# Kernel tuning notes

Hardware: AMD Instinct MI355X
Metric: run time of the kernel (lower is better)

The kernel has to match this reference:

```python
import jax, jax.numpy as jnp
import numpy as np

ANCHORS = [np.array([[10, 13], [16, 30], [33, 23]], np.float32),
           np.array([[30, 61], [62, 45], [59, 119]], np.float32),
           np.array([[116, 90], [156, 198], [373, 326]], np.float32)]
STRIDES = [8.0, 16.0, 32.0]
BALANCE = [4.0, 1.0, 0.4]
LAMBDA_OBJ, LAMBDA_CLS, LAMBDA_IOU = 1.0, 0.5, 1.0
NUM_CLASSES = 80
EPS = 1e-7


def _bce_logits(x, t):
    # numerically stable BCEWithLogits, reduction='none'
    return jnp.maximum(x, 0.0) - x * t + jnp.log1p(jnp.exp(-jnp.abs(x)))


def _ciou(box1, box2):
    # boxes in (cx, cy, w, h); standard ultralytics CIoU
    w1, h1 = box1[..., 2], box1[..., 3]
    w2, h2 = box2[..., 2], box2[..., 3]
    b1x1, b1x2 = box1[..., 0] - w1 / 2, box1[..., 0] + w1 / 2
    b1y1, b1y2 = box1[..., 1] - h1 / 2, box1[..., 1] + h1 / 2
    b2x1, b2x2 = box2[..., 0] - w2 / 2, box2[..., 0] + w2 / 2
    b2y1, b2y2 = box2[..., 1] - h2 / 2, box2[..., 1] + h2 / 2
    inter = (jnp.clip(jnp.minimum(b1x2, b2x2) - jnp.maximum(b1x1, b2x1), 0.0, None)
             * jnp.clip(jnp.minimum(b1y2, b2y2) - jnp.maximum(b1y1, b2y1), 0.0, None))
    union = w1 * h1 + w2 * h2 - inter + EPS
    iou = inter / union
    cw = jnp.maximum(b1x2, b2x2) - jnp.minimum(b1x1, b2x1)  # enclosing box
    ch = jnp.maximum(b1y2, b2y2) - jnp.minimum(b1y1, b2y1)
    c2 = cw ** 2 + ch ** 2 + EPS
    rho2 = ((b2x1 + b2x2 - b1x1 - b1x2) ** 2 + (b2y1 + b2y2 - b1y1 - b1y2) ** 2) / 4.0
    v = (4.0 / np.pi ** 2) * (jnp.arctan(w2 / (h2 + EPS)) - jnp.arctan(w1 / (h1 + EPS))) ** 2
    alpha = jax.lax.stop_gradient(v / (v - iou + 1.0 + EPS))
    return iou - (rho2 / c2 + v * alpha)


def _build_targets(boxes, labels, stride, anchors_wh, B, A, H, W, C):
    # Vectorized version of the torch per-gt loops: anchor shape matching +
    # scatter into dense target tensors. boxes [B,N,4] x1y1x2y2, labels [B,N].
    gt_xy = (boxes[..., :2] + boxes[..., 2:]) / 2.0          # [B,N,2]
    gt_wh = boxes[..., 2:] - boxes[..., :2]                  # [B,N,2]
    xy_grid = gt_xy / stride
    gi = jnp.clip(xy_grid[..., 1].astype(jnp.int32), 0, H - 1)
    gj = jnp.clip(xy_grid[..., 0].astype(jnp.int32), 0, W - 1)
    r = gt_wh[:, :, None, :] / anchors_wh[None, None, :, :]  # [B,N,A,2]
    shape_metric = jnp.maximum(r[..., 0], 1.0 / r[..., 0]) * jnp.maximum(r[..., 1], 1.0 / r[..., 1])
    best = jnp.argmax(1.0 / shape_metric, axis=-1)           # [B,N]
    tx = xy_grid[..., 0] - gj.astype(jnp.float32)
    ty = xy_grid[..., 1] - gi.astype(jnp.float32)
    aw = anchors_wh[best]                                    # [B,N,2]
    tw = jnp.log(gt_wh[..., 0] / (aw[..., 0] + 1e-16))
    th = jnp.log(gt_wh[..., 1] / (aw[..., 1] + 1e-16))
    bidx = jnp.broadcast_to(jnp.arange(B)[:, None], best.shape)
    obj = jnp.zeros((B, A, H, W), jnp.float32).at[bidx, best, gi, gj].set(1.0)
    tvals = jax.lax.stop_gradient(jnp.stack([tx, ty, tw, th], axis=-1))
    tbox = jnp.zeros((B, A, H, W, 4), jnp.float32).at[bidx, best, gi, gj].set(tvals)
    tcls = jnp.zeros((B, A, H, W, C), jnp.float32).at[bidx, best, gi, gj, labels].set(1.0)
    return obj, tbox, tcls


def _scale_loss(pred, boxes, labels, anchors_raw, stride, balance):
    B, _, H, W = pred.shape
    A = anchors_raw.shape[0]
    C = NUM_CLASSES
    p = pred.reshape(B, A, 5 + C, H, W).transpose(0, 1, 3, 4, 2)  # [B,A,H,W,5+C]
    pbox, pobj, pcls = p[..., :4], p[..., 4], p[..., 5:]
    gy, gx = jnp.meshgrid(jnp.arange(H, dtype=jnp.float32),
                          jnp.arange(W, dtype=jnp.float32), indexing='ij')
    grid = jnp.stack([gx, gy], axis=-1)                           # [H,W,2]
    anchors = jnp.asarray(anchors_raw)
    anchors_wh = anchors * stride                                  # pixel-space anchors
    pred_xy = (jax.nn.sigmoid(pbox[..., :2]) + grid) * stride
    pred_wh = jnp.exp(pbox[..., 2:]) * anchors_wh[None, :, None, None, :]
    pred_boxes = jnp.concatenate([pred_xy, pred_wh], axis=-1)      # cxcywh pixels
    obj, tbox, tcls = _build_targets(boxes, labels, stride, anchors_wh, B, A, H, W, C)
    npos = jnp.sum(obj)
    # decode target boxes back to cxcywh pixels (matches indices-based torch path)
    tgt_xy = (grid + tbox[..., :2]) * stride
    tgt_wh = jnp.exp(tbox[..., 2:]) * anchors_wh[None, :, None, None, :]
    tgt_boxes = jnp.concatenate([tgt_xy, tgt_wh], axis=-1)
    ciou = _ciou(pred_boxes, tgt_boxes)
    box_l = LAMBDA_IOU * jnp.sum((1.0 - ciou) * obj) / jnp.maximum(npos, 1.0)
    bce_obj = _bce_logits(pobj, obj)  # positive target = 1, negative target = 0
    obj_l = LAMBDA_OBJ * balance * (jnp.sum(bce_obj * obj) + 0.5 * jnp.sum(bce_obj * (1.0 - obj)))
    cls_l = LAMBDA_CLS * jnp.sum(_bce_logits(pcls, tcls) * obj[..., None])
    return box_l, obj_l, cls_l


def setup_inputs() -> dict:
    key = jax.random.key(0)
    k1, k2, k3, k4, k5, k6 = jax.random.split(key, 6)
    B, N, C, A = 16, 32, 80, 3
    ch = A * (5 + C)
    pred_small = jax.random.normal(k1, (B, ch, 80, 80), jnp.float32)
    pred_medium = jax.random.normal(k2, (B, ch, 40, 40), jnp.float32)
    pred_large = jax.random.normal(k3, (B, ch, 20, 20), jnp.float32)
    cxy = jax.random.uniform(k4, (B, N, 2), minval=32.0, maxval=608.0)
    wh = jax.random.uniform(k5, (B, N, 2), minval=8.0, maxval=256.0)
    boxes = jnp.concatenate([cxy - wh / 2, cxy + wh / 2], axis=-1)  # x1y1x2y2, 640px img
    labels = jax.random.randint(k6, (B, N), 0, C)
    return {"pred_small": pred_small, "pred_medium": pred_medium,
            "pred_large": pred_large, "boxes": boxes, "labels": labels}


def reference(pred_small, pred_medium, pred_large, boxes, labels):
    B = pred_small.shape[0]
    box_l = obj_l = cls_l = jnp.float32(0.0)
    for pred, anc, stride, bal in zip((pred_small, pred_medium, pred_large), ANCHORS, STRIDES, BALANCE):
        b, o, c = _scale_loss(pred, boxes, labels, anc, stride, bal)
        box_l, obj_l, cls_l = box_l + b, obj_l + o, cls_l + c
    total = (box_l + obj_l + cls_l) / B
    return total
```

## Files before the change

### kernel.cpp

```cpp
#include <hip/hip_runtime.h>
#include <math.h>

#define EPSF 1e-7f

__constant__ float c_anch[3][3][2] = {
    {{80.f,104.f},{128.f,240.f},{264.f,184.f}},
    {{480.f,976.f},{992.f,720.f},{944.f,1904.f}},
    {{3712.f,2880.f},{4992.f,6336.f},{11936.f,10432.f}}
};
__constant__ float c_stride[3] = {8.f, 16.f, 32.f};
__constant__ float c_bal[3]    = {4.f, 1.f, 0.4f};
__constant__ int   c_HW[3]     = {6400, 1600, 400};
__constant__ int   c_W[3]      = {80, 40, 20};

__device__ __forceinline__ float bce0(float x) {
    return fmaxf(x, 0.f) + __logf(1.f + __expf(-fabsf(x)));
}

__global__ __launch_bounds__(256) void fused_main(
        const float* __restrict__ p0, const float* __restrict__ p1,
        const float* __restrict__ p2,
        const float* __restrict__ boxes, const int* __restrict__ labels,
        float4* __restrict__ part, float* __restrict__ nposPart)
{
    __shared__ float red[4][4];

    const int bid  = blockIdx.x;
    const int tid  = threadIdx.x;
    const int lane = tid & 63, wv = tid >> 6;

    const bool isPos = (bid < 384);
    const int s   = bid >> 7;
    const int b   = (bid >> 3) & 15;
    const int grp = bid & 7;

    float4 bx; int labl = 0;
    if (isPos && lane < 32) {
        bx   = ((const float4*)boxes)[b * 32 + lane];
        labl = labels[b * 32 + lane];
    }

    float dsum = 0.f;
    {
        int v = bid * 252 + tid;
        if (tid < 252) {
            int sc, run, off, HW;
            const float* pred;
            if (v < 76800)      { sc = 0; HW = 6400; run = v / 1600;          off = v - run * 1600;         pred = p0; }
            else if (v < 96000) { sc = 1; HW = 1600; int u = v - 76800; run = u / 400; off = u - run * 400; pred = p1; }
            else                { sc = 2; HW = 400;  int u = v - 96000; run = u / 100; off = u - run * 100; pred = p2; }
            int bb = run / 3, a = run - bb * 3;
            const float4* ptr = (const float4*)(pred + (size_t)(bb * 255 + a * 85 + 4) * HW) + off;
            float4 x = *ptr;
            float w = 0.5f * c_bal[sc];
            dsum = w * (bce0(x.x) + bce0(x.y) + bce0(x.z) + bce0(x.w));
        }
    }

    float boxc = 0.f, objc = 0.f, clsp = 0.f;
    if (isPos) {
        int key = 0; float txl = 0.f, tyl = 0.f, twl = 0.f, thl = 0.f;
        {
            float cx = (bx.x + bx.z) * 0.5f, cy = (bx.y + bx.w) * 0.5f;
            float w  = bx.z - bx.x,          h  = bx.w - bx.y;
            float stride = c_stride[s];
            float xg = cx / stride, yg = cy / stride;
            int W = c_W[s];
            int gi = min(max((int)yg, 0), W - 1);
            int gj = min(max((int)xg, 0), W - 1);
            int best = 0; float bm = 1e30f;
            for (int k = 0; k < 3; ++k) {
                float aw = c_anch[s][k][0], ah = c_anch[s][k][1];
                float r0 = w / aw, r1 = h / ah;
                float m = fmaxf(r0, 1.f / r0) * fmaxf(r1, 1.f / r1);
                if (m < bm) { bm = m; best = k; }
            }
            float aw = c_anch[s][best][0], ah = c_anch[s][best][1];
            key = (best << 20) | (gi << 10) | gj;
            txl = xg - (float)gj;
            tyl = yg - (float)gi;
            twl = __logf(w / (aw + 1e-16f));
            thl = __logf(h / (ah + 1e-16f));
        }

        if (grp == 0 && wv == 0) {
            bool dup = false;
            for (int d = 1; d < 32; ++d) {
                int nk = __shfl(key, (lane + d) & 31);
                dup |= ((lane + d) < 32) && (nk == key);
            }
            bool winl = (lane < 32) && !dup;
            unsigned long long bal = __ballot(winl);
            if (lane == 0) nposPart[s * 16 + b] = (float)__popcll(bal);
        }

        const int n = grp * 4 + wv;
        int   key_n = __shfl(key, n);
        float tx_n  = __shfl(txl, n);
        float ty_n  = __shfl(tyl, n);
        float tw_n  = __shfl(twl, n);
        float th_n  = __shfl(thl, n);
        int   lab   = __shfl(labl, n);
        unsigned long long dupm =
            __ballot((lane > n) && (lane < 32) && (key == key_n));
        bool win = (dupm == 0ull);

        if (win) {
            int a  = key_n >> 20;
            int gi = (key_n >> 10) & 1023;
            int gj = key_n & 1023;
            const int HW = c_HW[s], W = c_W[s];
            int hw = gi * W + gj;
            const float* pred = (s == 0) ? p0 : ((s == 1) ? p1 : p2);
            const float* pb_ = pred + (size_t)(b * 255 + a * 85) * HW + hw;
            const float* pc  = pb_ + (size_t)5 * HW;

            float xc0 = pc[(size_t)lane * HW];
            float xc1 = (lane < 16) ? pc[(size_t)(lane + 64) * HW] : 0.f;
            clsp = bce0(xc0) - ((lane == lab) ? xc0 : 0.f);
            if (lane < 16) clsp += bce0(xc1) - ((lane + 64 == lab) ? xc1 : 0.f);

            float px = pb_[0], py = pb_[(size_t)HW];
            float pw = pb_[2 * (size_t)HW], ph = pb_[3 * (size_t)HW];
            float xo = pb_[4 * (size_t)HW];

            objc = c_bal[s] * (0.5f * bce0(xo) - xo);

            const float stride = c_stride[s];
            const float aw = c_anch[s][a][0], ah = c_anch[s][a][1];
            float sx = 1.f / (1.f + __expf(-px));
            float sy = 1.f / (1.f + __expf(-py));
            float b1x = (sx + (float)gj) * stride, b1y = (sy + (float)gi) * stride;
            float b1w = __expf(pw) * aw,           b1h = __expf(ph) * ah;
            float b2x = ((float)gj + tx_n) * stride, b2y = ((float)gi + ty_n) * stride;
            float b2w = __expf(tw_n) * aw,           b2h = __expf(th_n) * ah;

            float b1x1 = b1x - b1w * 0.5f, b1x2 = b1x + b1w * 0.5f;
            float b1y1 = b1y - b1h * 0.5f, b1y2 = b1y + b1h * 0.5f;
            float b2x1 = b2x - b2w * 0.5f, b2x2 = b2x + b2w * 0.5f;
            float b2y1 = b2y - b2h * 0.5f, b2y2 = b2y + b2h * 0.5f;
            float iw = fmaxf(fminf(b1x2, b2x2) - fmaxf(b1x1, b2x1), 0.f);
            float ih = fmaxf(fminf(b1y2, b2y2) - fmaxf(b1y1, b2y1), 0.f);
            float inter = iw * ih;
            float uni = b1w * b1h + b2w * b2h - inter + EPSF;
            float iou = inter / uni;
            float cwv = fmaxf(b1x2, b2x2) - fminf(b1x1, b2x1);
            float chv = fmaxf(b1y2, b2y2) - fminf(b1y1, b2y1);
            float c2 = cwv * cwv + chv * chv + EPSF;
            float dx = b2x1 + b2x2 - b1x1 - b1x2;
            float dy = b2y1 + b2y2 - b1y1 - b1y2;
            float rho2 = (dx * dx + dy * dy) * 0.25f;
            float dat = atanf(b2w / (b2h + EPSF)) - atanf(b1w / (b1h + EPSF));
            float v = (4.f / (float)(M_PI * M_PI)) * dat * dat;
            float alpha = v / (v - iou + 1.f + EPSF);
            boxc = 1.f - (iou - (rho2 / c2 + v * alpha));
        }
    }

    for (int o = 32; o > 0; o >>= 1) {
        dsum += __shfl_down(dsum, o);
        clsp += __shfl_down(clsp, o);
    }
    if (lane == 0) {
        red[wv][0] = dsum; red[wv][1] = boxc; red[wv][2] = objc; red[wv][3] = clsp;
    }
    __syncthreads();
    if (tid == 0) {
        float d = 0.f, bxs = 0.f, oc = 0.f, cl = 0.f;
        for (int i = 0; i < 4; ++i) {
            d += red[i][0]; bxs += red[i][1]; oc += red[i][2]; cl += red[i][3];
        }
        part[bid] = make_float4(bxs, d + oc, cl, 0.f);
    }
}

__global__ __launch_bounds__(256) void finalize(
        const float4* __restrict__ part, const float* __restrict__ nposPart,
        float* __restrict__ out)
{
    int tid = threadIdx.x;
    float bx0 = 0.f, bx1 = 0.f, bx2 = 0.f, obj = 0.f, cls = 0.f;
    for (int i = tid; i < 400; i += 256) {
        float4 p = part[i];
        obj += p.y;
        cls += p.z;
        int sc = i >> 7;
        bx0 += (sc == 0) ? p.x : 0.f;
        bx1 += (sc == 1) ? p.x : 0.f;
        bx2 += (sc == 2) ? p.x : 0.f;
    }
    float np0 = 0.f, np1 = 0.f, np2 = 0.f;
    if (tid < 48) {
        float v = nposPart[tid];
        int sc = tid / 16;
        np0 = (sc == 0) ? v : 0.f;
        np1 = (sc == 1) ? v : 0.f;
        np2 = (sc == 2) ? v : 0.f;
    }

    for (int o = 32; o > 0; o >>= 1) {
        bx0 += __shfl_down(bx0, o);
        bx1 += __shfl_down(bx1, o);
        bx2 += __shfl_down(bx2, o);
        obj += __shfl_down(obj, o);
        cls += __shfl_down(cls, o);
        np0 += __shfl_down(np0, o);
        np1 += __shfl_down(np1, o);
        np2 += __shfl_down(np2, o);
    }
    __shared__ float red[4][8];
    int wv = tid >> 6;
    if ((tid & 63) == 0) {
        red[wv][0] = bx0; red[wv][1] = bx1; red[wv][2] = bx2; red[wv][3] = obj;
        red[wv][4] = cls; red[wv][5] = np0; red[wv][6] = np1; red[wv][7] = np2;
    }
    __syncthreads();
    if (tid == 0) {
        float v[8];
        for (int j = 0; j < 8; ++j)
            v[j] = red[0][j] + red[1][j] + red[2][j] + red[3][j];
        float tot = v[0] / fmaxf(v[5], 1.f)
                  + v[1] / fmaxf(v[6], 1.f)
                  + v[2] / fmaxf(v[7], 1.f)
                  + v[3]
                  + 0.5f * v[4];
        out[0] = tot / 16.f;
    }
}

extern "C" void kernel_launch(void* const* d_in, const int* in_sizes, int n_in,
                              void* d_out, int out_size, void* d_ws, size_t ws_size,
                              hipStream_t stream)
{
    const float* p0     = (const float*)d_in[0];
    const float* p1     = (const float*)d_in[1];
    const float* p2     = (const float*)d_in[2];
    const float* boxes  = (const float*)d_in[3];
    const int*   labels = (const int*)d_in[4];

    char* ws = (char*)d_ws;
    float4* part     = (float4*)ws;
    float*  nposPart = (float*)(ws + 6656);

    fused_main<<<400, 256, 0, stream>>>(p0, p1, p2, boxes, labels,
                                        part, nposPart);
    finalize<<<1, 256, 0, stream>>>(part, nposPart, (float*)d_out);
}
```

Measured before the change: 12.12 us.

## Fuse finalize into main kernel via per-block npos recompute and atomicAdd

Removes the second finalize launch. Each positive block now recomputes the per-scale count of unique positive cells for all 16 images itself: each wave handles 4 images, two per half-wave, with redundant key building. Each block then adds its normalized contribution to the output with atomicAdd after a memset. This trades a kernel launch and an inter-kernel dependency for duplicated dedup work in every positive block, atomic contention on a single float, and a nondeterministic summation order.

Measured after the change: 20.23 us. 67.0% more time.

```diff
diff --git a/kernel.cpp b/kernel.cpp
--- a/kernel.cpp
+++ b/kernel.cpp
@@ -17,13 +17,30 @@
     return fmaxf(x, 0.f) + __logf(1.f + __expf(-fabsf(x)));
 }
 
-__global__ __launch_bounds__(256) void fused_main(
+__device__ __forceinline__ int buildKey(float4 bx, int s) {
+    float cx = (bx.x + bx.z) * 0.5f, cy = (bx.y + bx.w) * 0.5f;
+    float w  = bx.z - bx.x,          h  = bx.w - bx.y;
+    float stride = c_stride[s];
+    int W = c_W[s];
+    int gi = min(max((int)(cy / stride), 0), W - 1);
+    int gj = min(max((int)(cx / stride), 0), W - 1);
+    int best = 0; float bm = 1e30f;
+    for (int k = 0; k < 3; ++k) {
+        float aw = c_anch[s][k][0], ah = c_anch[s][k][1];
+        float r0 = w / aw, r1 = h / ah;
+        float m = fmaxf(r0, 1.f / r0) * fmaxf(r1, 1.f / r1);
+        if (m < bm) { bm = m; best = k; }
+    }
+    return (best << 20) | (gi << 10) | gj;
+}
+
+__global__ __launch_bounds__(256) void fused_all(
         const float* __restrict__ p0, const float* __restrict__ p1,
         const float* __restrict__ p2,
         const float* __restrict__ boxes, const int* __restrict__ labels,
-        float4* __restrict__ part, float* __restrict__ nposPart)
+        float* __restrict__ out)
 {
-    __shared__ float red[4][4];
+    __shared__ float red[4][5];
 
     const int bid  = blockIdx.x;
     const int tid  = threadIdx.x;
@@ -35,9 +52,14 @@
     const int grp = bid & 7;
 
     float4 bx; int labl = 0;
-    if (isPos && lane < 32) {
-        bx   = ((const float4*)boxes)[b * 32 + lane];
-        labl = labels[b * 32 + lane];
+    float4 bxn0, bxn1;
+    if (isPos) {
+        if (lane < 32) {
+            bx   = ((const float4*)boxes)[b * 32 + lane];
+            labl = labels[b * 32 + lane];
+        }
+        bxn0 = ((const float4*)boxes)[(wv * 4 + 0 + (lane >> 5)) * 32 + (lane & 31)];
+        bxn1 = ((const float4*)boxes)[(wv * 4 + 2 + (lane >> 5)) * 32 + (lane & 31)];
     }
 
     float dsum = 0.f;
@@ -58,7 +80,26 @@
     }
 
     float boxc = 0.f, objc = 0.f, clsp = 0.f;
+    float npw = 0.f;
     if (isPos) {
+        {
+            const int l32 = lane & 31, base = lane & 32;
+            int k0 = buildKey(bxn0, s);
+            bool dup = false;
+            for (int d = 1; d < 32; ++d) {
+                int nk = __shfl(k0, base + ((l32 + d) & 31));
+                dup |= ((l32 + d) < 32) && (nk == k0);
+            }
+            npw += (float)__popcll(__ballot(!dup));
+            int k1 = buildKey(bxn1, s);
+            dup = false;
+            for (int d = 1; d < 32; ++d) {
+                int nk = __shfl(k1, base + ((l32 + d) & 31));
+                dup |= ((l32 + d) < 32) && (nk == k1);
+            }
+            npw += (float)__popcll(__ballot(!dup));
+        }
+
         int key = 0; float txl = 0.f, tyl = 0.f, twl = 0.f, thl = 0.f;
         {
             float cx = (bx.x + bx.z) * 0.5f, cy = (bx.y + bx.w) * 0.5f;
@@ -83,17 +124,6 @@
             thl = __logf(h / (ah + 1e-16f));
         }
 
-        if (grp == 0 && wv == 0) {
-            bool dup = false;
-            for (int d = 1; d < 32; ++d) {
-                int nk = __shfl(key, (lane + d) & 31);
-                dup |= ((lane + d) < 32) && (nk == key);
-            }
-            bool winl = (lane < 32) && !dup;
-            unsigned long long bal = __ballot(winl);
-            if (lane == 0) nposPart[s * 16 + b] = (float)__popcll(bal);
-        }
-
         const int n = grp * 4 + wv;
         int   key_n = __shfl(key, n);
         float tx_n  = __shfl(txl, n);
@@ -162,69 +192,18 @@
         clsp += __shfl_down(clsp, o);
     }
     if (lane == 0) {
-        red[wv][0] = dsum; red[wv][1] = boxc; red[wv][2] = objc; red[wv][3] = clsp;
+        red[wv][0] = dsum; red[wv][1] = boxc; red[wv][2] = objc;
+        red[wv][3] = clsp; red[wv][4] = npw;
     }
     __syncthreads();
     if (tid == 0) {
-        float d = 0.f, bxs = 0.f, oc = 0.f, cl = 0.f;
+        float d = 0.f, bxs = 0.f, oc = 0.f, cl = 0.f, np = 0.f;
         for (int i = 0; i < 4; ++i) {
-            d += red[i][0]; bxs += red[i][1]; oc += red[i][2]; cl += red[i][3];
-        }
-        part[bid] = make_float4(bxs, d + oc, cl, 0.f);
-    }
-}
-
-__global__ __launch_bounds__(256) void finalize(
-        const float4* __restrict__ part, const float* __restrict__ nposPart,
-        float* __restrict__ out)
-{
-    int tid = threadIdx.x;
-    float bx0 = 0.f, bx1 = 0.f, bx2 = 0.f, obj = 0.f, cls = 0.f;
-    for (int i = tid; i < 400; i += 256) {
-        float4 p = part[i];
-        obj += p.y;
-        cls += p.z;
-        int sc = i >> 7;
-        bx0 += (sc == 0) ? p.x : 0.f;
-        bx1 += (sc == 1) ? p.x : 0.f;
-        bx2 += (sc == 2) ? p.x : 0.f;
-    }
-    float np0 = 0.f, np1 = 0.f, np2 = 0.f;
-    if (tid < 48) {
-        float v = nposPart[tid];
-        int sc = tid / 16;
-        np0 = (sc == 0) ? v : 0.f;
-        np1 = (sc == 1) ? v : 0.f;
-        np2 = (sc == 2) ? v : 0.f;
-    }
-
-    for (int o = 32; o > 0; o >>= 1) {
-        bx0 += __shfl_down(bx0, o);
-        bx1 += __shfl_down(bx1, o);
-        bx2 += __shfl_down(bx2, o);
-        obj += __shfl_down(obj, o);
-        cls += __shfl_down(cls, o);
-        np0 += __shfl_down(np0, o);
-        np1 += __shfl_down(np1, o);
-        np2 += __shfl_down(np2, o);
-    }
-    __shared__ float red[4][8];
-    int wv = tid >> 6;
-    if ((tid & 63) == 0) {
-        red[wv][0] = bx0; red[wv][1] = bx1; red[wv][2] = bx2; red[wv][3] = obj;
-        red[wv][4] = cls; red[wv][5] = np0; red[wv][6] = np1; red[wv][7] = np2;
-    }
-    __syncthreads();
-    if (tid == 0) {
-        float v[8];
-        for (int j = 0; j < 8; ++j)
-            v[j] = red[0][j] + red[1][j] + red[2][j] + red[3][j];
-        float tot = v[0] / fmaxf(v[5], 1.f)
-                  + v[1] / fmaxf(v[6], 1.f)
-                  + v[2] / fmaxf(v[7], 1.f)
-                  + v[3]
-                  + 0.5f * v[4];
-        out[0] = tot / 16.f;
+            d  += red[i][0]; bxs += red[i][1]; oc += red[i][2];
+            cl += red[i][3]; np  += red[i][4];
+        }
+        float contrib = d + oc + 0.5f * cl + bxs / fmaxf(np, 1.f);
+        atomicAdd(out, contrib * 0.0625f);
     }
 }
 
@@ -238,11 +217,8 @@
     const float* boxes  = (const float*)d_in[3];
     const int*   labels = (const int*)d_in[4];
 
-    char* ws = (char*)d_ws;
-    float4* part     = (float4*)ws;
-    float*  nposPart = (float*)(ws + 6656);
-
-    fused_main<<<400, 256, 0, stream>>>(p0, p1, p2, boxes, labels,
-                                        part, nposPart);
-    finalize<<<1, 256, 0, stream>>>(part, nposPart, (float*)d_out);
-}
+    hipMemsetAsync(d_out, 0, sizeof(float), stream);
+
+    fused_all<<<400, 256, 0, stream>>>(p0, p1, p2, boxes, labels,
+                                       (float*)d_out);
+}
```

## Fuse finalize into main kernel via last-block epoch-tagged spin wait

Applied to the files above, without the earlier changes.

Removes the separate finalize launch. Each block publishes its partials with agent-scope atomic stores and bumps a per-block tag with release semantics. Block 399 waits until every tag reaches the current epoch, then does the final reduction. This saves one kernel launch and its gap, but it relies on all 400 blocks being resident or completing before block 399 spins, and it adds atomic traffic.

Result: slower. 15.26 us (+25.9%).

```diff
diff --git a/kernel.cpp b/kernel.cpp
--- a/kernel.cpp
+++ b/kernel.cpp
@@ -13,17 +13,29 @@
 __constant__ int   c_HW[3]     = {6400, 1600, 400};
 __constant__ int   c_W[3]      = {80, 40, 20};
 
+__device__ unsigned int g_tag[400];
+__device__ unsigned int g_epoch;
+
 __device__ __forceinline__ float bce0(float x) {
     return fmaxf(x, 0.f) + __logf(1.f + __expf(-fabsf(x)));
 }
 
-__global__ __launch_bounds__(256) void fused_main(
+__device__ __forceinline__ void agent_store(float* p, float v) {
+    __hip_atomic_store(p, v, __ATOMIC_RELAXED, __HIP_MEMORY_SCOPE_AGENT);
+}
+__device__ __forceinline__ float agent_load(const float* p) {
+    return __hip_atomic_load(p, __ATOMIC_RELAXED, __HIP_MEMORY_SCOPE_AGENT);
+}
+
+__global__ __launch_bounds__(256) void fused_all(
         const float* __restrict__ p0, const float* __restrict__ p1,
         const float* __restrict__ p2,
         const float* __restrict__ boxes, const int* __restrict__ labels,
-        float4* __restrict__ part, float* __restrict__ nposPart)
+        float* __restrict__ part, float* __restrict__ nposPart,
+        float* __restrict__ out)
 {
-    __shared__ float red[4][4];
+    __shared__ float red[4][8];
+    __shared__ unsigned int sEpoch;
 
     const int bid  = blockIdx.x;
     const int tid  = threadIdx.x;
@@ -91,7 +103,7 @@
             }
             bool winl = (lane < 32) && !dup;
             unsigned long long bal = __ballot(winl);
-            if (lane == 0) nposPart[s * 16 + b] = (float)__popcll(bal);
+            if (lane == 0) agent_store(&nposPart[s * 16 + b], (float)__popcll(bal));
         }
 
         const int n = grp * 4 + wv;
@@ -170,28 +182,43 @@
         for (int i = 0; i < 4; ++i) {
             d += red[i][0]; bxs += red[i][1]; oc += red[i][2]; cl += red[i][3];
         }
-        part[bid] = make_float4(bxs, d + oc, cl, 0.f);
-    }
-}
-
-__global__ __launch_bounds__(256) void finalize(
-        const float4* __restrict__ part, const float* __restrict__ nposPart,
-        float* __restrict__ out)
-{
-    int tid = threadIdx.x;
+        float* dst = part + (size_t)bid * 4;
+        agent_store(dst + 0, bxs);
+        agent_store(dst + 1, d + oc);
+        agent_store(dst + 2, cl);
+        __hip_atomic_fetch_add(&g_tag[bid], 1u,
+                               __ATOMIC_RELEASE, __HIP_MEMORY_SCOPE_AGENT);
+    }
+
+    if (bid != 399) return;
+
+    if (tid == 0)
+        sEpoch = __hip_atomic_fetch_add(&g_epoch, 1u,
+                     __ATOMIC_RELAXED, __HIP_MEMORY_SCOPE_AGENT) + 1u;
+    __syncthreads();
+    const unsigned int epoch = sEpoch;
+    for (int i = tid; i < 400; i += 256) {
+        while ((int)(__hip_atomic_load(&g_tag[i], __ATOMIC_RELAXED,
+                                       __HIP_MEMORY_SCOPE_AGENT) - epoch) < 0)
+            __builtin_amdgcn_s_sleep(1);
+    }
+    __syncthreads();
+    __builtin_amdgcn_fence(__ATOMIC_ACQUIRE, "agent");
+
     float bx0 = 0.f, bx1 = 0.f, bx2 = 0.f, obj = 0.f, cls = 0.f;
     for (int i = tid; i < 400; i += 256) {
-        float4 p = part[i];
-        obj += p.y;
-        cls += p.z;
+        const float* src = part + (size_t)i * 4;
+        float bv = agent_load(src + 0);
+        obj += agent_load(src + 1);
+        cls += agent_load(src + 2);
         int sc = i >> 7;
-        bx0 += (sc == 0) ? p.x : 0.f;
-        bx1 += (sc == 1) ? p.x : 0.f;
-        bx2 += (sc == 2) ? p.x : 0.f;
+        bx0 += (sc == 0) ? bv : 0.f;
+        bx1 += (sc == 1) ? bv : 0.f;
+        bx2 += (sc == 2) ? bv : 0.f;
     }
     float np0 = 0.f, np1 = 0.f, np2 = 0.f;
     if (tid < 48) {
-        float v = nposPart[tid];
+        float v = agent_load(&nposPart[tid]);
         int sc = tid / 16;
         np0 = (sc == 0) ? v : 0.f;
         np1 = (sc == 1) ? v : 0.f;
@@ -208,9 +235,8 @@
         np1 += __shfl_down(np1, o);
         np2 += __shfl_down(np2, o);
     }
-    __shared__ float red[4][8];
-    int wv = tid >> 6;
-    if ((tid & 63) == 0) {
+    __syncthreads();
+    if (lane == 0) {
         red[wv][0] = bx0; red[wv][1] = bx1; red[wv][2] = bx2; red[wv][3] = obj;
         red[wv][4] = cls; red[wv][5] = np0; red[wv][6] = np1; red[wv][7] = np2;
     }
@@ -239,10 +265,9 @@
     const int*   labels = (const int*)d_in[4];
 
     char* ws = (char*)d_ws;
-    float4* part     = (float4*)ws;
-    float*  nposPart = (float*)(ws + 6656);
-
-    fused_main<<<400, 256, 0, stream>>>(p0, p1, p2, boxes, labels,
-                                        part, nposPart);
-    finalize<<<1, 256, 0, stream>>>(part, nposPart, (float*)d_out);
-}
+    float* part     = (float*)ws;
+    float* nposPart = (float*)(ws + 6656);
+
+    fused_all<<<400, 256, 0, stream>>>(p0, p1, p2, boxes, labels,
+                                       part, nposPart, (float*)d_out);
+}
```
